# Kernel tuning notes

Hardware: AMD Instinct MI355X
Metric: run time of the kernel (lower is better)

The kernel has to match this reference:

```python
import jax, jax.numpy as jnp
import numpy as np

NUM_CATS = 5
EPS = 1e-6


def setup_inputs() -> dict:
    key = jax.random.key(0)
    k1, k2, k3, k4 = jax.random.split(key, 4)
    B, C, H, W = 64, 3, 256, 256
    restored = jax.random.normal(k1, (B, C, H, W), dtype=jnp.float32)
    clean_patch_1 = jax.random.normal(k2, (B, C, H, W), dtype=jnp.float32)
    un = jax.random.uniform(k3, (B, C, H, W), dtype=jnp.float32)
    de_id = jax.random.randint(k4, (B,), 0, NUM_CATS)
    return {"restored": restored, "clean_patch_1": clean_patch_1,
            "de_id": de_id, "un": un}


def _loss(restored, clean, un, de_id):
    B, C, H, W = restored.shape
    E = C * H * W  # elements per sample
    dt = restored.dtype

    onehot = (de_id[:, None] == jnp.arange(NUM_CATS)[None, :])  # [B,5] bool
    m = onehot.astype(dt)                                        # [B,5]
    counts = onehot.sum(0)                                       # [5] int
    nonempty = counts > 0
    safe_counts = jnp.maximum(counts, 1).astype(dt)              # avoid 0-div

    # Per-category mean uncertainty map: un_map[c] = mean_{i: de_id[i]=c} un[i] + eps
    un_sum = jnp.einsum('bk,bchw->kchw', m, un)                  # [5,C,H,W]
    un_map = un_sum / safe_counts[:, None, None, None] + EPS     # [5,C,H,W]
    s = 1.0 / un_map                                             # [5,C,H,W]

    # Per-sample scaled L1 (s gathered by each sample's category)
    absdiff = jnp.abs(clean - restored)                          # [B,C,H,W]
    scaled_sum_per_sample = (absdiff * s[de_id]).sum(axis=(1, 2, 3))  # [B]
    abs_sum_per_sample = absdiff.sum(axis=(1, 2, 3))                  # [B]

    cat_scaled_sum = jnp.einsum('bk,b->k', m, scaled_sum_per_sample)  # [5]
    cat_abs_sum = jnp.einsum('bk,b->k', m, abs_sum_per_sample)        # [5]

    # NOTE: the original code never clears un_hq_list/un_lq_list between
    # categories, so the L1 at category c is the mean over ALL samples from
    # categories 0..c (each scaled by its OWN category's s). Replicate that
    # via cumulative sums/counts over the category axis.
    cum_scaled = jnp.cumsum(cat_scaled_sum)                      # [5]
    cum_elems = jnp.cumsum(counts).astype(dt) * E                # [5]
    cum_l1 = cum_scaled / jnp.maximum(cum_elems, 1.0)            # [5]

    old_loss = jnp.where(nonempty, cat_abs_sum / (safe_counts * E), 0.0)
    un_num = un_map.mean(axis=(1, 2, 3))                         # [5]
    bn = jnp.where(nonempty, 2.0 * jnp.log(un_num), 0.0)
    unc_l1 = jnp.where(nonempty, cum_l1, 0.0)

    cat_losses = unc_l1 + bn                                     # [5]
    num = nonempty.sum().astype(dt)
    total = cat_losses.sum() / num
    return total, cat_losses, old_loss, bn, unc_l1


def reference(restored, clean_patch_1, de_id, un):
    return _loss(restored, clean_patch_1, un, de_id)
```

## Files before the change

### kernel.cpp

```cpp
#include <hip/hip_runtime.h>
#include <math.h>

#define NCAT  5
#define BATCH 64
#define ELEMS 196608
#define NBLK  768
#define TPB   256
#define GRP   8
#define EPSV  1e-6f

__global__ __launch_bounds__(TPB) void accum_kernel(
    const float* __restrict__ restored,
    const float* __restrict__ clean,
    const int*   __restrict__ de_id,
    const float* __restrict__ un,
    float*       __restrict__ partials)
{
    __shared__ int   sh_de[BATCH];
    __shared__ float sh_inv[NCAT];
    __shared__ float sred[TPB / 64][3 * NCAT];

    const int tid = threadIdx.x;

    if (tid < 64) {
        int k = de_id[tid];
        sh_de[tid] = k;
        #pragma unroll
        for (int j = 0; j < NCAT; ++j) {
            unsigned long long m = __ballot(k == j);
            if (tid == j) {
                int c = __popcll(m);
                sh_inv[j] = 1.0f / (float)(c > 0 ? c : 1);
            }
        }
    }
    __syncthreads();

    const int p = blockIdx.x * TPB + tid;
    const float* rp = restored + p;
    const float* cp = clean + p;
    const float* up = un + p;

    float un_s[NCAT] = {0.f, 0.f, 0.f, 0.f, 0.f};
    float ad_s[NCAT] = {0.f, 0.f, 0.f, 0.f, 0.f};

    float ub[2][GRP], cb[2][GRP], rb[2][GRP];

    #pragma unroll
    for (int i = 0; i < GRP; ++i) {
        const size_t off = (size_t)i * ELEMS;
        ub[0][i] = up[off];
        cb[0][i] = cp[off];
        rb[0][i] = rp[off];
    }

    #pragma unroll
    for (int g = 0; g < BATCH / GRP; ++g) {
        const int cur = g & 1;
        const int nxt = cur ^ 1;
        if (g < BATCH / GRP - 1) {
            #pragma unroll
            for (int i = 0; i < GRP; ++i) {
                const size_t off = (size_t)((g + 1) * GRP + i) * ELEMS;
                ub[nxt][i] = up[off];
                cb[nxt][i] = cp[off];
                rb[nxt][i] = rp[off];
            }
        }
        #pragma unroll
        for (int i = 0; i < GRP; ++i) {
            float u  = ub[cur][i];
            float ad = fabsf(cb[cur][i] - rb[cur][i]);
            int   k  = sh_de[g * GRP + i];
            #pragma unroll
            for (int j = 0; j < NCAT; ++j) {
                float m = (k == j) ? 1.0f : 0.0f;
                un_s[j] = fmaf(m, u,  un_s[j]);
                ad_s[j] = fmaf(m, ad, ad_s[j]);
            }
        }
    }

    float vals[3 * NCAT];
    #pragma unroll
    for (int j = 0; j < NCAT; ++j) {
        float um = fmaf(un_s[j], sh_inv[j], EPSV);
        vals[j]            = ad_s[j] / um;
        vals[NCAT + j]     = ad_s[j];
        vals[2 * NCAT + j] = un_s[j];
    }

    #pragma unroll
    for (int i = 0; i < 3 * NCAT; ++i) {
        float v = vals[i];
        #pragma unroll
        for (int off = 32; off >= 1; off >>= 1)
            v += __shfl_down(v, off, 64);
        vals[i] = v;
    }

    const int wave = tid >> 6;
    const int lane = tid & 63;
    if (lane == 0) {
        #pragma unroll
        for (int i = 0; i < 3 * NCAT; ++i) sred[wave][i] = vals[i];
    }
    __syncthreads();

    if (tid < 3 * NCAT) {
        float v = sred[0][tid] + sred[1][tid] + sred[2][tid] + sred[3][tid];
        partials[tid * NBLK + blockIdx.x] = v;
    }
}

__global__ __launch_bounds__(256) void epilogue_kernel(
    const int*   __restrict__ de_id,
    const float* __restrict__ partials,
    float*       __restrict__ out)
{
    __shared__ int   sh_cnt[NCAT];
    __shared__ float sh_acc[3 * NCAT];

    const int tid = threadIdx.x;

    if (tid < 64) {
        int k = de_id[tid];
        #pragma unroll
        for (int j = 0; j < NCAT; ++j) {
            unsigned long long m = __ballot(k == j);
            if (tid == j) sh_cnt[j] = __popcll(m);
        }
    }

    if (tid < 240) {
        const int row    = tid >> 4;
        const int lane16 = tid & 15;
        float v = 0.f;
        #pragma unroll 4
        for (int k = 0; k < NBLK / 16; ++k)
            v += partials[row * NBLK + lane16 + (k << 4)];
        v += __shfl_down(v, 8, 16);
        v += __shfl_down(v, 4, 16);
        v += __shfl_down(v, 2, 16);
        v += __shfl_down(v, 1, 16);
        if (lane16 == 0) sh_acc[row] = v;
    }
    __syncthreads();

    if (tid == 0) {
        const float Ef = (float)ELEMS;
        float cum_s = 0.f;
        long  cum_c = 0;
        float total = 0.f;
        int   num   = 0;

        float cat_losses[NCAT], old_loss[NCAT], bn[NCAT], unc_l1[NCAT];

        for (int j = 0; j < NCAT; ++j) {
            cum_s += sh_acc[j];
            cum_c += sh_cnt[j];
            float cum_elems = (float)cum_c * Ef;
            float cum_l1    = cum_s / fmaxf(cum_elems, 1.0f);

            bool  ne   = sh_cnt[j] > 0;
            float safe = (float)(ne ? sh_cnt[j] : 1);

            old_loss[j]  = ne ? sh_acc[NCAT + j] / (safe * Ef) : 0.f;
            float un_num = sh_acc[2 * NCAT + j] / (safe * Ef) + EPSV;
            bn[j]        = ne ? 2.0f * logf(un_num) : 0.f;
            unc_l1[j]    = ne ? cum_l1 : 0.f;
            cat_losses[j] = unc_l1[j] + bn[j];
            total += cat_losses[j];
            num   += ne ? 1 : 0;
        }
        total /= (float)num;

        out[0] = total;
        for (int j = 0; j < NCAT; ++j) {
            out[1 + j]  = cat_losses[j];
            out[6 + j]  = old_loss[j];
            out[11 + j] = bn[j];
            out[16 + j] = unc_l1[j];
        }
    }
}

extern "C" void kernel_launch(void* const* d_in, const int* in_sizes, int n_in,
                              void* d_out, int out_size, void* d_ws, size_t ws_size,
                              hipStream_t stream) {
    (void)in_sizes; (void)n_in; (void)out_size; (void)ws_size;
    const float* restored = (const float*)d_in[0];
    const float* clean    = (const float*)d_in[1];
    const int*   de_id    = (const int*)d_in[2];
    const float* un       = (const float*)d_in[3];
    float* out      = (float*)d_out;
    float* partials = (float*)d_ws;

    accum_kernel<<<NBLK, TPB, 0, stream>>>(restored, clean, de_id, un, partials);
    epilogue_kernel<<<1, 256, 0, stream>>>(de_id, partials, out);
}
```

Baseline: 173.3 us.

## Split loss into uncertainty-map and batch-chunked L1 phases with float4 loads

Splits the single accumulation kernel into two phases. Phase one computes per-category mean uncertainty with float4 loads and writes the reciprocal map to workspace. Phase two splits the batch across a second grid dimension so many more blocks share the restored/clean stream, then applies the stored reciprocals. The aim is more memory-level parallelism and wider loads than the original 768-block kernel that walked all 64 samples per thread. In exchange it adds about 3.9 MB of extra map write and re-read traffic, an extra launch, and depends on the workspace being large enough, otherwise it falls back to the old path.

```diff
diff --git a/kernel.cpp b/kernel.cpp
--- a/kernel.cpp
+++ b/kernel.cpp
@@ -4,10 +4,195 @@
 #define NCAT  5
 #define BATCH 64
 #define ELEMS 196608
-#define NBLK  768
-#define TPB   256
-#define GRP   8
+#define P4    49152
 #define EPSV  1e-6f
+
+#define P1_TPB 64
+#define P1_NBLK 768
+#define P1_GRP 8
+
+#define P2_PB  192
+#define P2_SCH 8
+#define P2_CHB (BATCH / P2_SCH)
+#define P2_NCOL (P2_PB * P2_SCH)
+
+#define NBLK 768
+#define TPB  256
+#define GRP  8
+
+__global__ __launch_bounds__(P1_TPB) void phase1_kernel(
+    const float4* __restrict__ un,
+    const int*    __restrict__ de_id,
+    float4*       __restrict__ rmap,
+    float*        __restrict__ partials1)
+{
+    __shared__ int   sh_de[BATCH];
+    __shared__ float sh_inv[NCAT];
+
+    const int tid = threadIdx.x;
+    {
+        int k = de_id[tid];
+        sh_de[tid] = k;
+        #pragma unroll
+        for (int j = 0; j < NCAT; ++j) {
+            unsigned long long m = __ballot(k == j);
+            if (tid == j) {
+                int c = __popcll(m);
+                sh_inv[j] = 1.0f / (float)(c > 0 ? c : 1);
+            }
+        }
+    }
+    __syncthreads();
+
+    const int p4 = blockIdx.x * P1_TPB + tid;
+    const float4* up = un + p4;
+
+    float4 un_s[NCAT];
+    #pragma unroll
+    for (int j = 0; j < NCAT; ++j) un_s[j] = make_float4(0.f, 0.f, 0.f, 0.f);
+
+    float4 ub[2][P1_GRP];
+    #pragma unroll
+    for (int i = 0; i < P1_GRP; ++i) ub[0][i] = up[(size_t)i * P4];
+
+    #pragma unroll
+    for (int g = 0; g < BATCH / P1_GRP; ++g) {
+        const int cur = g & 1, nxt = cur ^ 1;
+        if (g < BATCH / P1_GRP - 1) {
+            #pragma unroll
+            for (int i = 0; i < P1_GRP; ++i)
+                ub[nxt][i] = up[(size_t)((g + 1) * P1_GRP + i) * P4];
+        }
+        #pragma unroll
+        for (int i = 0; i < P1_GRP; ++i) {
+            float4 u = ub[cur][i];
+            int k = sh_de[g * P1_GRP + i];
+            #pragma unroll
+            for (int j = 0; j < NCAT; ++j) {
+                float m = (k == j) ? 1.0f : 0.0f;
+                un_s[j].x = fmaf(m, u.x, un_s[j].x);
+                un_s[j].y = fmaf(m, u.y, un_s[j].y);
+                un_s[j].z = fmaf(m, u.z, un_s[j].z);
+                un_s[j].w = fmaf(m, u.w, un_s[j].w);
+            }
+        }
+    }
+
+    float vals[NCAT];
+    #pragma unroll
+    for (int j = 0; j < NCAT; ++j) {
+        float inv = sh_inv[j];
+        float4 r;
+        r.x = 1.0f / fmaf(un_s[j].x, inv, EPSV);
+        r.y = 1.0f / fmaf(un_s[j].y, inv, EPSV);
+        r.z = 1.0f / fmaf(un_s[j].z, inv, EPSV);
+        r.w = 1.0f / fmaf(un_s[j].w, inv, EPSV);
+        rmap[(size_t)j * P4 + p4] = r;
+        vals[j] = un_s[j].x + un_s[j].y + un_s[j].z + un_s[j].w;
+    }
+
+    #pragma unroll
+    for (int j = 0; j < NCAT; ++j) {
+        float v = vals[j];
+        #pragma unroll
+        for (int off = 32; off >= 1; off >>= 1)
+            v += __shfl_down(v, off, 64);
+        if (tid == 0) partials1[j * P1_NBLK + blockIdx.x] = v;
+    }
+}
+
+__global__ __launch_bounds__(256) void phase2_kernel(
+    const float4* __restrict__ restored,
+    const float4* __restrict__ clean,
+    const int*    __restrict__ de_id,
+    const float4* __restrict__ rmap,
+    float*        __restrict__ partials2)
+{
+    __shared__ int   sh_de[BATCH];
+    __shared__ float sred[4][2 * NCAT];
+
+    const int tid = threadIdx.x;
+    if (tid < 64) sh_de[tid] = de_id[tid];
+    __syncthreads();
+
+    const int p4 = blockIdx.x * 256 + tid;
+    const int b0 = blockIdx.y * P2_CHB;
+    const float4* cp = clean + p4;
+    const float4* rp = restored + p4;
+
+    float4 ad4[NCAT];
+    #pragma unroll
+    for (int j = 0; j < NCAT; ++j) ad4[j] = make_float4(0.f, 0.f, 0.f, 0.f);
+
+    float4 cb[2][2], rb[2][2];
+    #pragma unroll
+    for (int i = 0; i < 2; ++i) {
+        const size_t off = (size_t)(b0 + i) * P4;
+        cb[0][i] = cp[off];
+        rb[0][i] = rp[off];
+    }
+
+    #pragma unroll
+    for (int g = 0; g < P2_CHB / 2; ++g) {
+        const int cur = g & 1, nxt = cur ^ 1;
+        if (g < P2_CHB / 2 - 1) {
+            #pragma unroll
+            for (int i = 0; i < 2; ++i) {
+                const size_t off = (size_t)(b0 + (g + 1) * 2 + i) * P4;
+                cb[nxt][i] = cp[off];
+                rb[nxt][i] = rp[off];
+            }
+        }
+        #pragma unroll
+        for (int i = 0; i < 2; ++i) {
+            float4 c = cb[cur][i], r = rb[cur][i];
+            float ax = fabsf(c.x - r.x);
+            float ay = fabsf(c.y - r.y);
+            float az = fabsf(c.z - r.z);
+            float aw = fabsf(c.w - r.w);
+            int k = sh_de[b0 + g * 2 + i];
+            #pragma unroll
+            for (int j = 0; j < NCAT; ++j) {
+                float m = (k == j) ? 1.0f : 0.0f;
+                ad4[j].x = fmaf(m, ax, ad4[j].x);
+                ad4[j].y = fmaf(m, ay, ad4[j].y);
+                ad4[j].z = fmaf(m, az, ad4[j].z);
+                ad4[j].w = fmaf(m, aw, ad4[j].w);
+            }
+        }
+    }
+
+    float vals[2 * NCAT];
+    #pragma unroll
+    for (int j = 0; j < NCAT; ++j) {
+        float4 m4 = rmap[(size_t)j * P4 + p4];
+        vals[j] = ad4[j].x * m4.x + ad4[j].y * m4.y +
+                  ad4[j].z * m4.z + ad4[j].w * m4.w;
+        vals[NCAT + j] = ad4[j].x + ad4[j].y + ad4[j].z + ad4[j].w;
+    }
+
+    #pragma unroll
+    for (int i = 0; i < 2 * NCAT; ++i) {
+        float v = vals[i];
+        #pragma unroll
+        for (int off = 32; off >= 1; off >>= 1)
+            v += __shfl_down(v, off, 64);
+        vals[i] = v;
+    }
+
+    const int wave = tid >> 6, lane = tid & 63;
+    if (lane == 0) {
+        #pragma unroll
+        for (int i = 0; i < 2 * NCAT; ++i) sred[wave][i] = vals[i];
+    }
+    __syncthreads();
+
+    if (tid < 2 * NCAT) {
+        float v = sred[0][tid] + sred[1][tid] + sred[2][tid] + sred[3][tid];
+        const int col = blockIdx.y * P2_PB + blockIdx.x;
+        partials2[tid * P2_NCOL + col] = v;
+    }
+}
 
 __global__ __launch_bounds__(TPB) void accum_kernel(
     const float* __restrict__ restored,
@@ -21,7 +206,6 @@
     __shared__ float sred[TPB / 64][3 * NCAT];
 
     const int tid = threadIdx.x;
-
     if (tid < 64) {
         int k = de_id[tid];
         sh_de[tid] = k;
@@ -45,26 +229,19 @@
     float ad_s[NCAT] = {0.f, 0.f, 0.f, 0.f, 0.f};
 
     float ub[2][GRP], cb[2][GRP], rb[2][GRP];
-
     #pragma unroll
     for (int i = 0; i < GRP; ++i) {
         const size_t off = (size_t)i * ELEMS;
-        ub[0][i] = up[off];
-        cb[0][i] = cp[off];
-        rb[0][i] = rp[off];
-    }
-
+        ub[0][i] = up[off]; cb[0][i] = cp[off]; rb[0][i] = rp[off];
+    }
     #pragma unroll
     for (int g = 0; g < BATCH / GRP; ++g) {
-        const int cur = g & 1;
-        const int nxt = cur ^ 1;
+        const int cur = g & 1, nxt = cur ^ 1;
         if (g < BATCH / GRP - 1) {
             #pragma unroll
             for (int i = 0; i < GRP; ++i) {
                 const size_t off = (size_t)((g + 1) * GRP + i) * ELEMS;
-                ub[nxt][i] = up[off];
-                cb[nxt][i] = cp[off];
-                rb[nxt][i] = rp[off];
+                ub[nxt][i] = up[off]; cb[nxt][i] = cp[off]; rb[nxt][i] = rp[off];
             }
         }
         #pragma unroll
@@ -89,7 +266,6 @@
         vals[NCAT + j]     = ad_s[j];
         vals[2 * NCAT + j] = un_s[j];
     }
-
     #pragma unroll
     for (int i = 0; i < 3 * NCAT; ++i) {
         float v = vals[i];
@@ -98,15 +274,12 @@
             v += __shfl_down(v, off, 64);
         vals[i] = v;
     }
-
-    const int wave = tid >> 6;
-    const int lane = tid & 63;
+    const int wave = tid >> 6, lane = tid & 63;
     if (lane == 0) {
         #pragma unroll
         for (int i = 0; i < 3 * NCAT; ++i) sred[wave][i] = vals[i];
     }
     __syncthreads();
-
     if (tid < 3 * NCAT) {
         float v = sred[0][tid] + sred[1][tid] + sred[2][tid] + sred[3][tid];
         partials[tid * NBLK + blockIdx.x] = v;
@@ -115,14 +288,14 @@
 
 __global__ __launch_bounds__(256) void epilogue_kernel(
     const int*   __restrict__ de_id,
-    const float* __restrict__ partials,
+    const float* __restrict__ pSA, int nA,
+    const float* __restrict__ pUN, int nB,
     float*       __restrict__ out)
 {
     __shared__ int   sh_cnt[NCAT];
     __shared__ float sh_acc[3 * NCAT];
 
     const int tid = threadIdx.x;
-
     if (tid < 64) {
         int k = de_id[tid];
         #pragma unroll
@@ -135,10 +308,10 @@
     if (tid < 240) {
         const int row    = tid >> 4;
         const int lane16 = tid & 15;
+        const float* base = (row < 10) ? (pSA + row * nA) : (pUN + (row - 10) * nB);
+        const int n = (row < 10) ? nA : nB;
         float v = 0.f;
-        #pragma unroll 4
-        for (int k = 0; k < NBLK / 16; ++k)
-            v += partials[row * NBLK + lane16 + (k << 4)];
+        for (int k = lane16; k < n; k += 16) v += base[k];
         v += __shfl_down(v, 8, 16);
         v += __shfl_down(v, 4, 16);
         v += __shfl_down(v, 2, 16);
@@ -153,7 +326,6 @@
         long  cum_c = 0;
         float total = 0.f;
         int   num   = 0;
-
         float cat_losses[NCAT], old_loss[NCAT], bn[NCAT], unc_l1[NCAT];
 
         for (int j = 0; j < NCAT; ++j) {
@@ -188,14 +360,33 @@
 extern "C" void kernel_launch(void* const* d_in, const int* in_sizes, int n_in,
                               void* d_out, int out_size, void* d_ws, size_t ws_size,
                               hipStream_t stream) {
-    (void)in_sizes; (void)n_in; (void)out_size; (void)ws_size;
+    (void)in_sizes; (void)n_in; (void)out_size;
     const float* restored = (const float*)d_in[0];
     const float* clean    = (const float*)d_in[1];
     const int*   de_id    = (const int*)d_in[2];
     const float* un       = (const float*)d_in[3];
-    float* out      = (float*)d_out;
-    float* partials = (float*)d_ws;
-
-    accum_kernel<<<NBLK, TPB, 0, stream>>>(restored, clean, de_id, un, partials);
-    epilogue_kernel<<<1, 256, 0, stream>>>(de_id, partials, out);
-}
+    float* out = (float*)d_out;
+
+    const size_t rmap_bytes = (size_t)NCAT * P4 * sizeof(float4);
+    const size_t p1_bytes   = (size_t)NCAT * P1_NBLK * sizeof(float);
+    const size_t p2_bytes   = (size_t)2 * NCAT * P2_NCOL * sizeof(float);
+
+    if (ws_size >= rmap_bytes + p1_bytes + p2_bytes) {
+        float4* rmap      = (float4*)d_ws;
+        float*  partials1 = (float*)((char*)d_ws + rmap_bytes);
+        float*  partials2 = (float*)((char*)d_ws + rmap_bytes + p1_bytes);
+
+        phase1_kernel<<<P1_NBLK, P1_TPB, 0, stream>>>(
+            (const float4*)un, de_id, rmap, partials1);
+        phase2_kernel<<<dim3(P2_PB, P2_SCH), 256, 0, stream>>>(
+            (const float4*)restored, (const float4*)clean, de_id,
+            (const float4*)rmap, partials2);
+        epilogue_kernel<<<1, 256, 0, stream>>>(
+            de_id, partials2, P2_NCOL, partials1, P1_NBLK, out);
+    } else {
+        float* partials = (float*)d_ws;
+        accum_kernel<<<NBLK, TPB, 0, stream>>>(restored, clean, de_id, un, partials);
+        epilogue_kernel<<<1, 256, 0, stream>>>(
+            de_id, partials, NBLK, partials + 10 * NBLK, NBLK, out);
+    }
+}
```

After: 190.1 us. +9.7%, slower.

## Use float4 loads and split batch across lane groups with shuffle merge

Applied to the files above, without the earlier changes.

Each thread now handles four consecutive pixels through float4 loads, and the 64 batch samples are split across four 16-lane groups within a wave, each group covering 16 samples. Per-category uncertainty sums are merged across the groups with xor shuffles before the reciprocal is taken. This widens memory transactions and shortens each thread's serial dependency chain over the batch, at the cost of more cross-lane shuffles and reciprocals in the epilogue. The grid keeps the same 768 blocks of 256 threads.

```diff
diff --git a/kernel.cpp b/kernel.cpp
--- a/kernel.cpp
+++ b/kernel.cpp
@@ -4,21 +4,20 @@
 #define NCAT  5
 #define BATCH 64
 #define ELEMS 196608
+#define P4    49152
 #define NBLK  768
-#define TPB   256
-#define GRP   8
 #define EPSV  1e-6f
 
-__global__ __launch_bounds__(TPB) void accum_kernel(
-    const float* __restrict__ restored,
-    const float* __restrict__ clean,
-    const int*   __restrict__ de_id,
-    const float* __restrict__ un,
-    float*       __restrict__ partials)
+__global__ __launch_bounds__(256) void accum_kernel(
+    const float4* __restrict__ restored,
+    const float4* __restrict__ clean,
+    const int*    __restrict__ de_id,
+    const float4* __restrict__ un,
+    float*        __restrict__ partials)
 {
     __shared__ int   sh_de[BATCH];
     __shared__ float sh_inv[NCAT];
-    __shared__ float sred[TPB / 64][3 * NCAT];
+    __shared__ float sred[4][3 * NCAT];
 
     const int tid = threadIdx.x;
 
@@ -36,47 +35,66 @@
     }
     __syncthreads();
 
-    const int p = blockIdx.x * TPB + tid;
-    const float* rp = restored + p;
-    const float* cp = clean + p;
-    const float* up = un + p;
-
-    float un_s[NCAT] = {0.f, 0.f, 0.f, 0.f, 0.f};
-    float ad_s[NCAT] = {0.f, 0.f, 0.f, 0.f, 0.f};
-
-    float ub[2][GRP], cb[2][GRP], rb[2][GRP];
-
-    #pragma unroll
-    for (int i = 0; i < GRP; ++i) {
-        const size_t off = (size_t)i * ELEMS;
+    const int lane = tid & 63;
+    const int wave = tid >> 6;
+    const int grp  = lane >> 4;
+    const int posl = lane & 15;
+    const int p4   = blockIdx.x * 64 + wave * 16 + posl;
+    const int b0   = grp * 16;
+
+    const float4* rp = restored + p4;
+    const float4* cp = clean + p4;
+    const float4* up = un + p4;
+
+    float4 un_s[NCAT], ad_s[NCAT];
+    #pragma unroll
+    for (int j = 0; j < NCAT; ++j) {
+        un_s[j] = make_float4(0.f, 0.f, 0.f, 0.f);
+        ad_s[j] = make_float4(0.f, 0.f, 0.f, 0.f);
+    }
+
+    float4 ub[2][4], cb[2][4], rb[2][4];
+    #pragma unroll
+    for (int i = 0; i < 4; ++i) {
+        const size_t off = (size_t)(b0 + i) * P4;
         ub[0][i] = up[off];
         cb[0][i] = cp[off];
         rb[0][i] = rp[off];
     }
 
     #pragma unroll
-    for (int g = 0; g < BATCH / GRP; ++g) {
-        const int cur = g & 1;
-        const int nxt = cur ^ 1;
-        if (g < BATCH / GRP - 1) {
+    for (int st = 0; st < 4; ++st) {
+        const int cur = st & 1, nxt = cur ^ 1;
+        if (st < 3) {
             #pragma unroll
-            for (int i = 0; i < GRP; ++i) {
-                const size_t off = (size_t)((g + 1) * GRP + i) * ELEMS;
+            for (int i = 0; i < 4; ++i) {
+                const size_t off = (size_t)(b0 + (st + 1) * 4 + i) * P4;
                 ub[nxt][i] = up[off];
                 cb[nxt][i] = cp[off];
                 rb[nxt][i] = rp[off];
             }
         }
         #pragma unroll
-        for (int i = 0; i < GRP; ++i) {
-            float u  = ub[cur][i];
-            float ad = fabsf(cb[cur][i] - rb[cur][i]);
-            int   k  = sh_de[g * GRP + i];
+        for (int i = 0; i < 4; ++i) {
+            float4 u = ub[cur][i];
+            float4 c = cb[cur][i];
+            float4 r = rb[cur][i];
+            float ax = fabsf(c.x - r.x);
+            float ay = fabsf(c.y - r.y);
+            float az = fabsf(c.z - r.z);
+            float aw = fabsf(c.w - r.w);
+            int k = sh_de[b0 + st * 4 + i];
             #pragma unroll
             for (int j = 0; j < NCAT; ++j) {
                 float m = (k == j) ? 1.0f : 0.0f;
-                un_s[j] = fmaf(m, u,  un_s[j]);
-                ad_s[j] = fmaf(m, ad, ad_s[j]);
+                un_s[j].x = fmaf(m, u.x, un_s[j].x);
+                un_s[j].y = fmaf(m, u.y, un_s[j].y);
+                un_s[j].z = fmaf(m, u.z, un_s[j].z);
+                un_s[j].w = fmaf(m, u.w, un_s[j].w);
+                ad_s[j].x = fmaf(m, ax, ad_s[j].x);
+                ad_s[j].y = fmaf(m, ay, ad_s[j].y);
+                ad_s[j].z = fmaf(m, az, ad_s[j].z);
+                ad_s[j].w = fmaf(m, aw, ad_s[j].w);
             }
         }
     }
@@ -84,10 +102,23 @@
     float vals[3 * NCAT];
     #pragma unroll
     for (int j = 0; j < NCAT; ++j) {
-        float um = fmaf(un_s[j], sh_inv[j], EPSV);
-        vals[j]            = ad_s[j] / um;
-        vals[NCAT + j]     = ad_s[j];
-        vals[2 * NCAT + j] = un_s[j];
+        vals[2 * NCAT + j] = un_s[j].x + un_s[j].y + un_s[j].z + un_s[j].w;
+
+        float sx = un_s[j].x, sy = un_s[j].y, sz = un_s[j].z, sw = un_s[j].w;
+        sx += __shfl_xor(sx, 16, 64);  sx += __shfl_xor(sx, 32, 64);
+        sy += __shfl_xor(sy, 16, 64);  sy += __shfl_xor(sy, 32, 64);
+        sz += __shfl_xor(sz, 16, 64);  sz += __shfl_xor(sz, 32, 64);
+        sw += __shfl_xor(sw, 16, 64);  sw += __shfl_xor(sw, 32, 64);
+
+        const float inv = sh_inv[j];
+        float rx = 1.0f / fmaf(sx, inv, EPSV);
+        float ry = 1.0f / fmaf(sy, inv, EPSV);
+        float rz = 1.0f / fmaf(sz, inv, EPSV);
+        float rw = 1.0f / fmaf(sw, inv, EPSV);
+
+        vals[j] = ad_s[j].x * rx + ad_s[j].y * ry +
+                  ad_s[j].z * rz + ad_s[j].w * rw;
+        vals[NCAT + j] = ad_s[j].x + ad_s[j].y + ad_s[j].z + ad_s[j].w;
     }
 
     #pragma unroll
@@ -99,8 +130,6 @@
         vals[i] = v;
     }
 
-    const int wave = tid >> 6;
-    const int lane = tid & 63;
     if (lane == 0) {
         #pragma unroll
         for (int i = 0; i < 3 * NCAT; ++i) sred[wave][i] = vals[i];
@@ -122,7 +151,6 @@
     __shared__ float sh_acc[3 * NCAT];
 
     const int tid = threadIdx.x;
-
     if (tid < 64) {
         int k = de_id[tid];
         #pragma unroll
@@ -153,7 +181,6 @@
         long  cum_c = 0;
         float total = 0.f;
         int   num   = 0;
-
         float cat_losses[NCAT], old_loss[NCAT], bn[NCAT], unc_l1[NCAT];
 
         for (int j = 0; j < NCAT; ++j) {
@@ -189,13 +216,13 @@
                               void* d_out, int out_size, void* d_ws, size_t ws_size,
                               hipStream_t stream) {
     (void)in_sizes; (void)n_in; (void)out_size; (void)ws_size;
-    const float* restored = (const float*)d_in[0];
-    const float* clean    = (const float*)d_in[1];
-    const int*   de_id    = (const int*)d_in[2];
-    const float* un       = (const float*)d_in[3];
+    const float4* restored = (const float4*)d_in[0];
+    const float4* clean    = (const float4*)d_in[1];
+    const int*    de_id    = (const int*)d_in[2];
+    const float4* un       = (const float4*)d_in[3];
     float* out      = (float*)d_out;
     float* partials = (float*)d_ws;
 
-    accum_kernel<<<NBLK, TPB, 0, stream>>>(restored, clean, de_id, un, partials);
+    accum_kernel<<<NBLK, 256, 0, stream>>>(restored, clean, de_id, un, partials);
     epilogue_kernel<<<1, 256, 0, stream>>>(de_id, partials, out);
 }
```

New measurement: 174.8 us. Within noise of the previous version (+0.9%).
